# Performance work log

Measured on AMD Instinct MI355X. Metric: run time of the kernel, lower is better.

Reference implementation:

```python
import jax, jax.numpy as jnp
import numpy as np

C = 256
NUM_HEADS = 4
GROUPS = 8
EPS = 1e-5


def setup_inputs() -> dict:
    key = jax.random.key(0)
    ks = jax.random.split(key, 7)
    B, H, W = 4, 64, 64
    x = jax.random.normal(ks[0], (B, C, H, W), dtype=jnp.float32)
    # GroupNorm affine params
    norm_w = jnp.ones((C,), dtype=jnp.float32)
    norm_b = jnp.zeros((C,), dtype=jnp.float32)
    # 1x1 convs == channel-mixing matrices
    qkv_w = jax.random.normal(ks[1], (3 * C, C), dtype=jnp.float32) * (C ** -0.5)
    qkv_b = jnp.zeros((3 * C,), dtype=jnp.float32)
    proj_w = jax.random.normal(ks[2], (C, C), dtype=jnp.float32) * (C ** -0.5)
    proj_b = jnp.zeros((C,), dtype=jnp.float32)
    return {"x": x, "norm_w": norm_w, "norm_b": norm_b,
            "qkv_w": qkv_w, "qkv_b": qkv_b,
            "proj_w": proj_w, "proj_b": proj_b}


def _group_norm(x, w, b):
    B, Cc, H, W = x.shape
    xr = x.reshape(B, GROUPS, Cc // GROUPS, H * W)
    mean = xr.mean(axis=(2, 3), keepdims=True)
    var = xr.var(axis=(2, 3), keepdims=True)
    xn = ((xr - mean) * jax.lax.rsqrt(var + EPS)).reshape(B, Cc, H, W)
    return xn * w[None, :, None, None] + b[None, :, None, None]


def reference(x, norm_w, norm_b, qkv_w, qkv_b, proj_w, proj_b):
    B, Cc, H, W = x.shape
    nh = NUM_HEADS
    d = Cc // nh
    h = _group_norm(x, norm_w, norm_b)
    # 1x1 conv: channel matmul
    qkv = jnp.einsum('oc,bchw->bohw', qkv_w, h) + qkv_b[None, :, None, None]
    q, k, v = jnp.split(qkv, 3, axis=1)
    q = q.reshape(B, nh, d, H * W)
    k = k.reshape(B, nh, d, H * W)
    v = v.reshape(B, nh, d, H * W)
    scale = d ** -0.5
    attn = jnp.einsum('bhci,bhcj->bhij', q, k) * scale  # [B, nh, HW, HW]
    attn = jax.nn.softmax(attn, axis=-1)
    o = jnp.einsum('bhij,bhcj->bhci', attn, v).reshape(B, Cc, H, W)
    out = jnp.einsum('oc,bchw->bohw', proj_w, o) + proj_b[None, :, None, None]
    return x + out
```

## Files before the change

### kernel.cpp

```cpp
#include <hip/hip_runtime.h>

typedef unsigned short u16;
typedef __attribute__((ext_vector_type(8))) short bf16x8;
typedef __attribute__((ext_vector_type(16))) float f32x16;
typedef __attribute__((ext_vector_type(2))) int i32x2;

#define MFMA32(A, B, C) __builtin_amdgcn_mfma_f32_32x32x16_bf16((A), (B), (C), 0, 0, 0)
#define MFMA16(A, B, C) __builtin_amdgcn_mfma_f32_16x16x32_bf16((A), (B), (C), 0, 0, 0)

#define BB 4
#define CC 256
#define HW 4096
#define NH 4
#define HD 64

#define QSCALE 0.18033688f

typedef __attribute__((ext_vector_type(4))) float f32x4;

__device__ __forceinline__ u16 f2bf(float f) {
  unsigned int u = __builtin_bit_cast(unsigned int, f);
  u += 0x7fffu + ((u >> 16) & 1u);
  return (u16)(u >> 16);
}

__device__ __forceinline__ unsigned cvtpk(float a, float b) {
  unsigned r;
  asm("v_cvt_pk_bf16_f32 %0, %1, %2" : "=v"(r) : "v"(a), "v"(b));
  return r;
}

__device__ __forceinline__ uint4 pack_oct(const f32x16& a, int oct, float scl) {
  const int b8 = oct * 8;
  unsigned A0 = cvtpk(a[b8 + 0] * scl, a[b8 + 1] * scl);
  unsigned A1 = cvtpk(a[b8 + 2] * scl, a[b8 + 3] * scl);
  unsigned B0 = cvtpk(a[b8 + 4] * scl, a[b8 + 5] * scl);
  unsigned B1 = cvtpk(a[b8 + 6] * scl, a[b8 + 7] * scl);
  i32x2 r0 = __builtin_amdgcn_permlane32_swap((int)A0, (int)B0, false, false);
  i32x2 r1 = __builtin_amdgcn_permlane32_swap((int)A1, (int)B1, false, false);
  union { unsigned w[4]; uint4 v; } u;
  u.w[0] = (unsigned)r0[0]; u.w[1] = (unsigned)r1[0];
  u.w[2] = (unsigned)r0[1]; u.w[3] = (unsigned)r1[1];
  return u.v;
}

__global__ __launch_bounds__(256) void w2bf_kernel(const float* __restrict__ qw,
                                                   const float* __restrict__ pw,
                                                   u16* __restrict__ wbf) {
  int idx = (blockIdx.x * 256 + threadIdx.x) * 4;
  const int NQ = 768 * 256;
  const float* src = (idx < NQ) ? (qw + idx) : (pw + (idx - NQ));
  float4 v = *(const float4*)src;
  union { u16 u[4]; uint2 w; } pk;
  pk.u[0] = f2bf(v.x); pk.u[1] = f2bf(v.y);
  pk.u[2] = f2bf(v.z); pk.u[3] = f2bf(v.w);
  *(uint2*)(wbf + idx) = pk.w;
}

__global__ __launch_bounds__(256) void gn_partial_kernel(const float* __restrict__ x,
                                                         float* __restrict__ partial) {
  const float4* p = (const float4*)(x + (size_t)blockIdx.x * 16384);
  float s = 0.f, ss = 0.f;
  for (int i = threadIdx.x; i < 4096; i += 256) {
    float4 v = p[i];
    s += (v.x + v.y) + (v.z + v.w);
    ss += (v.x * v.x + v.y * v.y) + (v.z * v.z + v.w * v.w);
  }
#pragma unroll
  for (int msk = 32; msk; msk >>= 1) {
    s += __shfl_xor(s, msk);
    ss += __shfl_xor(ss, msk);
  }
  __shared__ float red[2][4];
  int wave = threadIdx.x >> 6;
  if ((threadIdx.x & 63) == 0) { red[0][wave] = s; red[1][wave] = ss; }
  __syncthreads();
  if (threadIdx.x == 0) {
    partial[blockIdx.x] = red[0][0] + red[0][1] + red[0][2] + red[0][3];
    partial[256 + blockIdx.x] = red[1][0] + red[1][1] + red[1][2] + red[1][3];
  }
}

__global__ __launch_bounds__(64) void gn_final_kernel(const float* __restrict__ partial,
                                                      float* __restrict__ stats) {
  int bg = threadIdx.x;
  if (bg < 32) {
    float S = 0.f, SS = 0.f;
#pragma unroll
    for (int sp = 0; sp < 8; ++sp) {
      S += partial[bg * 8 + sp];
      SS += partial[256 + bg * 8 + sp];
    }
    const float invN = 1.0f / 131072.0f;
    float mean = S * invN;
    float var = SS * invN - mean * mean;
    stats[bg] = mean;
    stats[32 + bg] = rsqrtf(var + 1e-5f);
  }
}

__global__ __launch_bounds__(256) void norm_t_kernel(const float* __restrict__ x,
                                                     const float* __restrict__ nw,
                                                     const float* __restrict__ nb,
                                                     const float* __restrict__ stats,
                                                     u16* __restrict__ h_t) {
  int b = blockIdx.y;
  int s = blockIdx.x * 64 + (threadIdx.x & 63);
  int w = threadIdx.x >> 6;
  const float* xb = x + (size_t)b * CC * HW;
  u16* hb = h_t + ((size_t)b * HW + s) * CC;
#pragma unroll
  for (int cc = 0; cc < 8; ++cc) {
    int c0 = w * 64 + cc * 8;
    union { u16 u[8]; uint4 v; } pk;
#pragma unroll
    for (int j = 0; j < 8; ++j) {
      int c = c0 + j;
      int g = c >> 5;
      float mean = stats[b * 8 + g];
      float rstd = stats[32 + b * 8 + g];
      float a = nw[c] * rstd;
      float bb2 = nb[c] - mean * a;
      float vv = xb[(size_t)c * HW + s];
      pk.u[j] = f2bf(vv * a + bb2);
    }
    *(uint4*)(hb + c0) = pk.v;
  }
}

__global__ __launch_bounds__(256) void qkv_kernel(const u16* __restrict__ h_t,
                                                  const u16* __restrict__ wbf,
                                                  const float* __restrict__ qb,
                                                  u16* __restrict__ q_f,
                                                  u16* __restrict__ k_f,
                                                  u16* __restrict__ v_f) {
  int b = blockIdx.z;
  int y = blockIdx.y;
  int lane = threadIdx.x & 63, wave = threadIdx.x >> 6;
  int ql = lane & 31, hi = lane >> 5;
  int s0w = blockIdx.x * 128 + (wave >> 1) * 64;
  int o0w = y * 128 + (wave & 1) * 64;
  bool isV = (y >= 4);
  const u16* hb = h_t + (size_t)b * HW * CC;

  f32x16 acc[2][2];
  if (!isV) {
#pragma unroll
    for (int mo = 0; mo < 2; ++mo)
#pragma unroll
      for (int r = 0; r < 16; ++r) {
        int row = (r & 3) + 8 * (r >> 2) + 4 * hi;
        float bv = qb[o0w + mo * 32 + row];
        acc[mo][0][r] = bv;
        acc[mo][1][r] = bv;
      }
  } else {
#pragma unroll
    for (int ns = 0; ns < 2; ++ns) {
      float bv = qb[o0w + ns * 32 + ql];
#pragma unroll
      for (int r = 0; r < 16; ++r) {
        acc[0][ns][r] = bv;
        acc[1][ns][r] = bv;
      }
    }
  }

  for (int kk = 0; kk < 16; ++kk) {
    int k0 = kk * 16 + hi * 8;
    bf16x8 wf[2], hf[2];
#pragma unroll
    for (int t = 0; t < 2; ++t) {
      wf[t] = *(const bf16x8*)(wbf + (size_t)(o0w + t * 32 + ql) * CC + k0);
      hf[t] = *(const bf16x8*)(hb + (size_t)(s0w + t * 32 + ql) * CC + k0);
    }
    if (!isV) {
      acc[0][0] = MFMA32(wf[0], hf[0], acc[0][0]);
      acc[0][1] = MFMA32(wf[0], hf[1], acc[0][1]);
      acc[1][0] = MFMA32(wf[1], hf[0], acc[1][0]);
      acc[1][1] = MFMA32(wf[1], hf[1], acc[1][1]);
    } else {
      acc[0][0] = MFMA32(hf[0], wf[0], acc[0][0]);
      acc[0][1] = MFMA32(hf[0], wf[1], acc[0][1]);
      acc[1][0] = MFMA32(hf[1], wf[0], acc[1][0]);
      acc[1][1] = MFMA32(hf[1], wf[1], acc[1][1]);
    }
  }

  if (!isV) {
    bool isQ = (y < 2);
    float scl = isQ ? QSCALE : 1.0f;
    int headL = (o0w >> 6) - (isQ ? 0 : 4);
    u16* base = (isQ ? q_f : k_f) + (size_t)(b * NH + headL) * HW * HD;
#pragma unroll
    for (int mo = 0; mo < 2; ++mo)
#pragma unroll
      for (int ns = 0; ns < 2; ++ns) {
        int s32 = (s0w >> 5) + ns;
#pragma unroll
        for (int oct = 0; oct < 2; ++oct) {
          int kc = mo * 2 + oct;
          uint4 v = pack_oct(acc[mo][ns], oct, scl);
          *(uint4*)(base + ((size_t)(s32 * 4 + kc) * 64 + lane) * 8) = v;
        }
      }
  } else {
    int headv = (o0w >> 6) - 8;
    u16* base = v_f + (size_t)(b * NH + headv) * HW * HD;
#pragma unroll
    for (int mo = 0; mo < 2; ++mo)
#pragma unroll
      for (int ns = 0; ns < 2; ++ns)
#pragma unroll
        for (int oct = 0; oct < 2; ++oct) {
          int kvb = s0w + mo * 32 + oct * 16;
          int jb64 = kvb >> 6, kcv = (kvb & 63) >> 4;
          uint4 v = pack_oct(acc[mo][ns], oct, 1.0f);
          *(uint4*)(base + ((size_t)((jb64 * 2 + ns) * 4 + kcv) * 64 + lane) * 8) = v;
        }
  }
}

__global__ __launch_bounds__(512) void attn_kernel(const u16* __restrict__ q_f,
                                                   const u16* __restrict__ k_f,
                                                   const u16* __restrict__ v_f,
                                                   u16* __restrict__ o_t) {
  __shared__ float mbuf[4 * 33 * 64];
  int wgid = blockIdx.x + gridDim.x * blockIdx.y;
  int xcd = wgid & 7;
  int j = wgid >> 3;
  int bh = (xcd << 1) | (j & 1);
  int qblk = j >> 1;
  int tid = threadIdx.x;
  int wave = tid >> 6, lane = tid & 63;
  int half = wave >> 2, wsub = wave & 3;
  int ql = lane & 31, hi = lane >> 5;
  int q0w = qblk * 128 + wsub * 32;
  const u16* qfb = q_f + (size_t)bh * HW * HD + lane * 8;
  const u16* kfb = k_f + (size_t)bh * HW * HD + lane * 8;
  const u16* vfb = v_f + (size_t)bh * HW * HD + lane * 8;

  int s32q = q0w >> 5;
  bf16x8 qf[4];
#pragma unroll
  for (int kc = 0; kc < 4; ++kc)
    qf[kc] = *(const bf16x8*)(qfb + (size_t)(s32q * 4 + kc) * 512);

  float l_run = 0.f;
  f32x16 of0 = {}, of1 = {};
  bf16x8 kfr[8], vfr[8];

  {
    const u16* kb = kfb + (size_t)half * 4096;
    const u16* vb = vfb + (size_t)half * 4096;
#pragma unroll
    for (int kc = 0; kc < 4; ++kc) {
      kfr[kc] = *(const bf16x8*)(kb + (size_t)kc * 512);
      kfr[4 + kc] = *(const bf16x8*)(kb + (size_t)(4 + kc) * 512);
      vfr[kc] = *(const bf16x8*)(vb + (size_t)kc * 512);
      vfr[4 + kc] = *(const bf16x8*)(vb + (size_t)(4 + kc) * 512);
    }
  }

#pragma unroll 1
  for (int it = half; it < 64; it += 2) {
    f32x16 s0 = {}, s1 = {};
    __builtin_amdgcn_s_setprio(1);
#pragma unroll
    for (int kc = 0; kc < 4; ++kc) {
      s0 = MFMA32(kfr[kc], qf[kc], s0);
      s1 = MFMA32(kfr[4 + kc], qf[kc], s1);
    }
    __builtin_amdgcn_s_setprio(0);

    {
      const u16* kb = kfb + (size_t)(it + 2) * 4096;
#pragma unroll
      for (int kc = 0; kc < 4; ++kc) {
        kfr[kc] = *(const bf16x8*)(kb + (size_t)kc * 512);
        kfr[4 + kc] = *(const bf16x8*)(kb + (size_t)(4 + kc) * 512);
      }
    }

#pragma unroll
    for (int i = 0; i < 16; ++i) {
      s0[i] = __builtin_amdgcn_exp2f(s0[i]);
      s1[i] = __builtin_amdgcn_exp2f(s1[i]);
    }

    bf16x8 pf[4];
#pragma unroll
    for (int kc = 0; kc < 4; ++kc) {
      const f32x16 pv = (kc < 2) ? s0 : s1;
      const int b8 = (kc & 1) * 8;
      unsigned A0 = cvtpk(pv[b8 + 0], pv[b8 + 1]);
      unsigned A1 = cvtpk(pv[b8 + 2], pv[b8 + 3]);
      unsigned B0 = cvtpk(pv[b8 + 4], pv[b8 + 5]);
      unsigned B1 = cvtpk(pv[b8 + 6], pv[b8 + 7]);
      i32x2 r0 = __builtin_amdgcn_permlane32_swap((int)A0, (int)B0, false, false);
      i32x2 r1 = __builtin_amdgcn_permlane32_swap((int)A1, (int)B1, false, false);
      union { unsigned w[4]; bf16x8 v8; } u;
      u.w[0] = (unsigned)r0[0]; u.w[1] = (unsigned)r1[0];
      u.w[2] = (unsigned)r0[1]; u.w[3] = (unsigned)r1[1];
      pf[kc] = u.v8;
    }

    __builtin_amdgcn_s_setprio(1);
#pragma unroll
    for (int kc = 0; kc < 4; ++kc) {
      of0 = MFMA32(vfr[kc], pf[kc], of0);
      of1 = MFMA32(vfr[4 + kc], pf[kc], of1);
    }
    __builtin_amdgcn_s_setprio(0);

    {
      const u16* vb = vfb + (size_t)(it + 2) * 4096;
#pragma unroll
      for (int kc = 0; kc < 4; ++kc) {
        vfr[kc] = *(const bf16x8*)(vb + (size_t)kc * 512);
        vfr[4 + kc] = *(const bf16x8*)(vb + (size_t)(4 + kc) * 512);
      }
    }

    float t8[8];
#pragma unroll
    for (int i = 0; i < 8; ++i)
      t8[i] = (s0[i] + s0[i + 8]) + (s1[i] + s1[i + 8]);
    float t4a = t8[0] + t8[4], t4b = t8[1] + t8[5];
    float t4c = t8[2] + t8[6], t4d = t8[3] + t8[7];
    l_run += (t4a + t4b) + (t4c + t4d);
  }

  __syncthreads();
  if (half == 1) {
    float* mb = mbuf + (size_t)wsub * 33 * 64 + lane;
#pragma unroll
    for (int i = 0; i < 16; ++i) mb[i * 64] = of0[i];
#pragma unroll
    for (int i = 0; i < 16; ++i) mb[(16 + i) * 64] = of1[i];
    mb[32 * 64] = l_run;
  }
  __syncthreads();
  if (half == 0) {
    const float* mb = mbuf + (size_t)wsub * 33 * 64 + lane;
#pragma unroll
    for (int i = 0; i < 16; ++i) of0[i] += mb[i * 64];
#pragma unroll
    for (int i = 0; i < 16; ++i) of1[i] += mb[(16 + i) * 64];
    l_run += mb[32 * 64];
    float l_tot = l_run + __shfl_xor(l_run, 32);
    float inv_l = 1.0f / l_tot;
    int bb = bh >> 2, hh = bh & 3;
    u16* orow = o_t + ((size_t)bb * HW + q0w + ql) * CC + hh * 64;
#pragma unroll
    for (int cb = 0; cb < 2; ++cb) {
      const f32x16 o = cb ? of1 : of0;
#pragma unroll
      for (int t = 0; t < 4; ++t) {
        int c0 = cb * 32 + t * 8 + hi * 4;
        union { u16 u[4]; uint2 w; } pk;
#pragma unroll
        for (int r = 0; r < 4; ++r) pk.u[r] = f2bf(o[t * 4 + r] * inv_l);
        *(uint2*)(orow + c0) = pk.w;
      }
    }
  }
}

__global__ __launch_bounds__(256) void proj_kernel(const u16* __restrict__ o_t,
                                                   const u16* __restrict__ wbf,
                                                   const float* __restrict__ pb,
                                                   const float* __restrict__ x,
                                                   float* __restrict__ out) {
  int b = blockIdx.z;
  int lane = threadIdx.x & 63, wave = threadIdx.x >> 6;
  int lr = lane & 15, lg = lane >> 4;
  int m0 = blockIdx.x * 128 + (wave >> 1) * 64;
  int n0 = blockIdx.y * 128 + (wave & 1) * 64;
  const u16* ob = o_t + (size_t)b * HW * CC;
  const u16* pwbf = wbf + (size_t)768 * CC;
  f32x4 acc[4][4] = {};
  for (int kc = 0; kc < 8; ++kc) {
    int ko = kc * 32 + lg * 8;
    bf16x8 af[4], bfr[4];
#pragma unroll
    for (int mi = 0; mi < 4; ++mi)
      af[mi] = *(const bf16x8*)(ob + (size_t)(m0 + mi * 16 + lr) * CC + ko);
#pragma unroll
    for (int ni = 0; ni < 4; ++ni)
      bfr[ni] = *(const bf16x8*)(pwbf + (size_t)(n0 + ni * 16 + lr) * CC + ko);
#pragma unroll
    for (int mi = 0; mi < 4; ++mi)
#pragma unroll
      for (int ni = 0; ni < 4; ++ni)
        acc[mi][ni] = MFMA16(af[mi], bfr[ni], acc[mi][ni]);
  }
#pragma unroll
  for (int ni = 0; ni < 4; ++ni) {
    int o = n0 + ni * 16 + lr;
    float bias = pb[o];
    const float* xp = x + ((size_t)b * CC + o) * HW;
    float* op = out + ((size_t)b * CC + o) * HW;
#pragma unroll
    for (int mi = 0; mi < 4; ++mi) {
      int sb = m0 + mi * 16 + lg * 4;
      float4 xv = *(const float4*)(xp + sb);
      float4 res;
      res.x = acc[mi][ni][0] + bias + xv.x;
      res.y = acc[mi][ni][1] + bias + xv.y;
      res.z = acc[mi][ni][2] + bias + xv.z;
      res.w = acc[mi][ni][3] + bias + xv.w;
      *(float4*)(op + sb) = res;
    }
  }
}

extern "C" void kernel_launch(void* const* d_in, const int* in_sizes, int n_in,
                              void* d_out, int out_size, void* d_ws, size_t ws_size,
                              hipStream_t stream) {
  const float* x = (const float*)d_in[0];
  const float* nw = (const float*)d_in[1];
  const float* nb = (const float*)d_in[2];
  const float* qw = (const float*)d_in[3];
  const float* qb = (const float*)d_in[4];
  const float* pw = (const float*)d_in[5];
  const float* pb = (const float*)d_in[6];
  float* out = (float*)d_out;

  float* stats = (float*)d_ws;
  float* partial = stats + 64;
  u16* h_t = (u16*)((char*)d_ws + 4096);
  u16* q_f = h_t + (size_t)BB * HW * CC;
  u16* k_f = q_f + (size_t)BB * HW * CC;
  u16* v_f = k_f + (size_t)BB * HW * CC;
  u16* wbf = v_f + (size_t)BB * HW * CC;
  u16* o_t = h_t;

  gn_partial_kernel<<<256, 256, 0, stream>>>(x, partial);
  gn_final_kernel<<<1, 64, 0, stream>>>(partial, stats);
  w2bf_kernel<<<256, 256, 0, stream>>>(qw, pw, wbf);
  norm_t_kernel<<<dim3(HW / 64, BB), 256, 0, stream>>>(x, nw, nb, stats, h_t);
  qkv_kernel<<<dim3(HW / 128, 6, BB), 256, 0, stream>>>(h_t, wbf, qb, q_f, k_f, v_f);
  attn_kernel<<<dim3(HW / 128, BB * NH), 512, 0, stream>>>(q_f, k_f, v_f, o_t);
  proj_kernel<<<dim3(HW / 128, 2, BB), 256, 0, stream>>>(o_t, wbf, pb, x, out);
}
```

Before: 154.5 us.

## Store weights, normalized input, and attention output in MFMA fragment layout

Weights, the normalized activations and the attention output are now written in a pre-swizzled per-lane MFMA fragment layout, so the qkv and proj GEMMs read contiguous 1KB chunks per wave instead of strided rows. norm_t now goes through an LDS transpose, and attention writes its output with packed 16-byte stores. proj switches from 16x16 to 32x32 MFMA and does a scalar-per-lane residual epilogue. The cost is more complex index math, and the proj epilogue now uses 4-byte rather than float4 stores.

```diff
diff --git a/kernel.cpp b/kernel.cpp
--- a/kernel.cpp
+++ b/kernel.cpp
@@ -6,7 +6,6 @@
 typedef __attribute__((ext_vector_type(2))) int i32x2;
 
 #define MFMA32(A, B, C) __builtin_amdgcn_mfma_f32_32x32x16_bf16((A), (B), (C), 0, 0, 0)
-#define MFMA16(A, B, C) __builtin_amdgcn_mfma_f32_16x16x32_bf16((A), (B), (C), 0, 0, 0)
 
 #define BB 4
 #define CC 256
@@ -15,8 +14,6 @@
 #define HD 64
 
 #define QSCALE 0.18033688f
-
-typedef __attribute__((ext_vector_type(4))) float f32x4;
 
 __device__ __forceinline__ u16 f2bf(float f) {
   unsigned int u = __builtin_bit_cast(unsigned int, f);
@@ -46,15 +43,19 @@
 
 __global__ __launch_bounds__(256) void w2bf_kernel(const float* __restrict__ qw,
                                                    const float* __restrict__ pw,
-                                                   u16* __restrict__ wbf) {
-  int idx = (blockIdx.x * 256 + threadIdx.x) * 4;
-  const int NQ = 768 * 256;
-  const float* src = (idx < NQ) ? (qw + idx) : (pw + (idx - NQ));
-  float4 v = *(const float4*)src;
-  union { u16 u[4]; uint2 w; } pk;
-  pk.u[0] = f2bf(v.x); pk.u[1] = f2bf(v.y);
-  pk.u[2] = f2bf(v.z); pk.u[3] = f2bf(v.w);
-  *(uint2*)(wbf + idx) = pk.w;
+                                                   u16* __restrict__ w_f) {
+  int wv = (blockIdx.x * 256 + threadIdx.x) >> 6;
+  int lane = threadIdx.x & 63;
+  int row = (wv >> 4) * 32 + (lane & 31);
+  int c0 = (wv & 15) * 16 + (lane >> 5) * 8;
+  const float* src = (row < 768) ? (qw + (size_t)row * 256 + c0)
+                                 : (pw + (size_t)(row - 768) * 256 + c0);
+  float4 a = *(const float4*)src;
+  float4 b = *(const float4*)(src + 4);
+  union { u16 u[8]; uint4 v; } pk;
+  pk.u[0] = f2bf(a.x); pk.u[1] = f2bf(a.y); pk.u[2] = f2bf(a.z); pk.u[3] = f2bf(a.w);
+  pk.u[4] = f2bf(b.x); pk.u[5] = f2bf(b.y); pk.u[6] = f2bf(b.z); pk.u[7] = f2bf(b.w);
+  *(uint4*)(w_f + ((size_t)wv * 64 + lane) * 8) = pk.v;
 }
 
 __global__ __launch_bounds__(256) void gn_partial_kernel(const float* __restrict__ x,
@@ -103,33 +104,39 @@
                                                      const float* __restrict__ nw,
                                                      const float* __restrict__ nb,
                                                      const float* __restrict__ stats,
-                                                     u16* __restrict__ h_t) {
+                                                     u16* __restrict__ h_f) {
+  __shared__ u16 L[256][66];
   int b = blockIdx.y;
-  int s = blockIdx.x * 64 + (threadIdx.x & 63);
-  int w = threadIdx.x >> 6;
+  int s0 = blockIdx.x * 64;
+  int lane = threadIdx.x & 63, w = threadIdx.x >> 6;
   const float* xb = x + (size_t)b * CC * HW;
-  u16* hb = h_t + ((size_t)b * HW + s) * CC;
-#pragma unroll
-  for (int cc = 0; cc < 8; ++cc) {
-    int c0 = w * 64 + cc * 8;
+  for (int cc = 0; cc < 64; ++cc) {
+    int c = w * 64 + cc;
+    int g = c >> 5;
+    float mean = stats[b * 8 + g];
+    float rstd = stats[32 + b * 8 + g];
+    float a = nw[c] * rstd;
+    float b2 = nb[c] - mean * a;
+    float v = xb[(size_t)c * HW + s0 + lane];
+    L[c][lane] = f2bf(v * a + b2);
+  }
+  __syncthreads();
+  u16* hb = h_f + (size_t)b * HW * CC;
+  int ql = lane & 31, hi = lane >> 5;
+  for (int t = w; t < 32; t += 4) {
+    int s32t = t >> 4, kc = t & 15;
+    int c0 = kc * 16 + hi * 8;
+    int s = s32t * 32 + ql;
     union { u16 u[8]; uint4 v; } pk;
 #pragma unroll
-    for (int j = 0; j < 8; ++j) {
-      int c = c0 + j;
-      int g = c >> 5;
-      float mean = stats[b * 8 + g];
-      float rstd = stats[32 + b * 8 + g];
-      float a = nw[c] * rstd;
-      float bb2 = nb[c] - mean * a;
-      float vv = xb[(size_t)c * HW + s];
-      pk.u[j] = f2bf(vv * a + bb2);
-    }
-    *(uint4*)(hb + c0) = pk.v;
-  }
-}
-
-__global__ __launch_bounds__(256) void qkv_kernel(const u16* __restrict__ h_t,
-                                                  const u16* __restrict__ wbf,
+    for (int j = 0; j < 8; ++j) pk.u[j] = L[c0 + j][s];
+    int s32g = (s0 >> 5) + s32t;
+    *(uint4*)(hb + ((size_t)(s32g * 16 + kc) * 64 + lane) * 8) = pk.v;
+  }
+}
+
+__global__ __launch_bounds__(256) void qkv_kernel(const u16* __restrict__ h_f,
+                                                  const u16* __restrict__ w_f,
                                                   const float* __restrict__ qb,
                                                   u16* __restrict__ q_f,
                                                   u16* __restrict__ k_f,
@@ -141,7 +148,7 @@
   int s0w = blockIdx.x * 128 + (wave >> 1) * 64;
   int o0w = y * 128 + (wave & 1) * 64;
   bool isV = (y >= 4);
-  const u16* hb = h_t + (size_t)b * HW * CC;
+  const u16* hb = h_f + (size_t)b * HW * CC;
 
   f32x16 acc[2][2];
   if (!isV) {
@@ -166,13 +173,13 @@
     }
   }
 
+  int os32 = o0w >> 5, ss32 = s0w >> 5;
   for (int kk = 0; kk < 16; ++kk) {
-    int k0 = kk * 16 + hi * 8;
     bf16x8 wf[2], hf[2];
 #pragma unroll
     for (int t = 0; t < 2; ++t) {
-      wf[t] = *(const bf16x8*)(wbf + (size_t)(o0w + t * 32 + ql) * CC + k0);
-      hf[t] = *(const bf16x8*)(hb + (size_t)(s0w + t * 32 + ql) * CC + k0);
+      wf[t] = *(const bf16x8*)(w_f + ((size_t)((os32 + t) * 16 + kk) * 64 + lane) * 8);
+      hf[t] = *(const bf16x8*)(hb + ((size_t)((ss32 + t) * 16 + kk) * 64 + lane) * 8);
     }
     if (!isV) {
       acc[0][0] = MFMA32(wf[0], hf[0], acc[0][0]);
@@ -196,7 +203,7 @@
     for (int mo = 0; mo < 2; ++mo)
 #pragma unroll
       for (int ns = 0; ns < 2; ++ns) {
-        int s32 = (s0w >> 5) + ns;
+        int s32 = ss32 + ns;
 #pragma unroll
         for (int oct = 0; oct < 2; ++oct) {
           int kc = mo * 2 + oct;
@@ -224,7 +231,7 @@
 __global__ __launch_bounds__(512) void attn_kernel(const u16* __restrict__ q_f,
                                                    const u16* __restrict__ k_f,
                                                    const u16* __restrict__ v_f,
-                                                   u16* __restrict__ o_t) {
+                                                   u16* __restrict__ o_f) {
   __shared__ float mbuf[4 * 33 * 64];
   int wgid = blockIdx.x + gridDim.x * blockIdx.y;
   int xcd = wgid & 7;
@@ -351,68 +358,68 @@
     float l_tot = l_run + __shfl_xor(l_run, 32);
     float inv_l = 1.0f / l_tot;
     int bb = bh >> 2, hh = bh & 3;
-    u16* orow = o_t + ((size_t)bb * HW + q0w + ql) * CC + hh * 64;
+    u16* obase = o_f + (size_t)bb * HW * CC;
+    int q32 = q0w >> 5;
 #pragma unroll
     for (int cb = 0; cb < 2; ++cb) {
       const f32x16 o = cb ? of1 : of0;
 #pragma unroll
-      for (int t = 0; t < 4; ++t) {
-        int c0 = cb * 32 + t * 8 + hi * 4;
-        union { u16 u[4]; uint2 w; } pk;
-#pragma unroll
-        for (int r = 0; r < 4; ++r) pk.u[r] = f2bf(o[t * 4 + r] * inv_l);
-        *(uint2*)(orow + c0) = pk.w;
-      }
-    }
-  }
-}
-
-__global__ __launch_bounds__(256) void proj_kernel(const u16* __restrict__ o_t,
-                                                   const u16* __restrict__ wbf,
+      for (int oct = 0; oct < 2; ++oct) {
+        int ck = hh * 4 + cb * 2 + oct;
+        uint4 v = pack_oct(o, oct, inv_l);
+        *(uint4*)(obase + ((size_t)(q32 * 16 + ck) * 64 + lane) * 8) = v;
+      }
+    }
+  }
+}
+
+__global__ __launch_bounds__(256) void proj_kernel(const u16* __restrict__ o_f,
+                                                   const u16* __restrict__ w_f,
                                                    const float* __restrict__ pb,
                                                    const float* __restrict__ x,
                                                    float* __restrict__ out) {
   int b = blockIdx.z;
   int lane = threadIdx.x & 63, wave = threadIdx.x >> 6;
-  int lr = lane & 15, lg = lane >> 4;
-  int m0 = blockIdx.x * 128 + (wave >> 1) * 64;
-  int n0 = blockIdx.y * 128 + (wave & 1) * 64;
-  const u16* ob = o_t + (size_t)b * HW * CC;
-  const u16* pwbf = wbf + (size_t)768 * CC;
-  f32x4 acc[4][4] = {};
-  for (int kc = 0; kc < 8; ++kc) {
-    int ko = kc * 32 + lg * 8;
-    bf16x8 af[4], bfr[4];
-#pragma unroll
-    for (int mi = 0; mi < 4; ++mi)
-      af[mi] = *(const bf16x8*)(ob + (size_t)(m0 + mi * 16 + lr) * CC + ko);
-#pragma unroll
-    for (int ni = 0; ni < 4; ++ni)
-      bfr[ni] = *(const bf16x8*)(pwbf + (size_t)(n0 + ni * 16 + lr) * CC + ko);
-#pragma unroll
-    for (int mi = 0; mi < 4; ++mi)
-#pragma unroll
-      for (int ni = 0; ni < 4; ++ni)
-        acc[mi][ni] = MFMA16(af[mi], bfr[ni], acc[mi][ni]);
-  }
-#pragma unroll
-  for (int ni = 0; ni < 4; ++ni) {
-    int o = n0 + ni * 16 + lr;
-    float bias = pb[o];
-    const float* xp = x + ((size_t)b * CC + o) * HW;
-    float* op = out + ((size_t)b * CC + o) * HW;
-#pragma unroll
-    for (int mi = 0; mi < 4; ++mi) {
-      int sb = m0 + mi * 16 + lg * 4;
-      float4 xv = *(const float4*)(xp + sb);
-      float4 res;
-      res.x = acc[mi][ni][0] + bias + xv.x;
-      res.y = acc[mi][ni][1] + bias + xv.y;
-      res.z = acc[mi][ni][2] + bias + xv.z;
-      res.w = acc[mi][ni][3] + bias + xv.w;
-      *(float4*)(op + sb) = res;
-    }
-  }
+  int ql = lane & 31, hi = lane >> 5;
+  int s0w = blockIdx.x * 128 + (wave >> 1) * 64;
+  int o0w = blockIdx.y * 128 + (wave & 1) * 64;
+  const u16* ob = o_f + (size_t)b * HW * CC;
+
+  f32x16 acc[2][2];
+#pragma unroll
+  for (int mo = 0; mo < 2; ++mo)
+#pragma unroll
+    for (int r = 0; r < 16; ++r) {
+      int row = (r & 3) + 8 * (r >> 2) + 4 * hi;
+      float bv = pb[o0w + mo * 32 + row];
+      acc[mo][0][r] = bv;
+      acc[mo][1][r] = bv;
+    }
+
+  int os32 = 24 + (o0w >> 5), ss32 = s0w >> 5;
+  for (int kk = 0; kk < 16; ++kk) {
+    bf16x8 af[2], bf2[2];
+#pragma unroll
+    for (int t = 0; t < 2; ++t) {
+      af[t] = *(const bf16x8*)(w_f + ((size_t)((os32 + t) * 16 + kk) * 64 + lane) * 8);
+      bf2[t] = *(const bf16x8*)(ob + ((size_t)((ss32 + t) * 16 + kk) * 64 + lane) * 8);
+    }
+    acc[0][0] = MFMA32(af[0], bf2[0], acc[0][0]);
+    acc[0][1] = MFMA32(af[0], bf2[1], acc[0][1]);
+    acc[1][0] = MFMA32(af[1], bf2[0], acc[1][0]);
+    acc[1][1] = MFMA32(af[1], bf2[1], acc[1][1]);
+  }
+
+#pragma unroll
+  for (int mo = 0; mo < 2; ++mo)
+#pragma unroll
+    for (int r = 0; r < 16; ++r) {
+      int o = o0w + mo * 32 + (r & 3) + 8 * (r >> 2) + 4 * hi;
+      const float* xp = x + ((size_t)b * CC + o) * HW + s0w + ql;
+      float* op = out + ((size_t)b * CC + o) * HW + s0w + ql;
+      op[0] = acc[mo][0][r] + xp[0];
+      op[32] = acc[mo][1][r] + xp[32];
+    }
 }
 
 extern "C" void kernel_launch(void* const* d_in, const int* in_sizes, int n_in,
@@ -429,18 +436,18 @@
 
   float* stats = (float*)d_ws;
   float* partial = stats + 64;
-  u16* h_t = (u16*)((char*)d_ws + 4096);
-  u16* q_f = h_t + (size_t)BB * HW * CC;
+  u16* h_f = (u16*)((char*)d_ws + 4096);
+  u16* q_f = h_f + (size_t)BB * HW * CC;
   u16* k_f = q_f + (size_t)BB * HW * CC;
   u16* v_f = k_f + (size_t)BB * HW * CC;
-  u16* wbf = v_f + (size_t)BB * HW * CC;
-  u16* o_t = h_t;
+  u16* w_f = v_f + (size_t)BB * HW * CC;
+  u16* o_f = h_f;
 
   gn_partial_kernel<<<256, 256, 0, stream>>>(x, partial);
   gn_final_kernel<<<1, 64, 0, stream>>>(partial, stats);
-  w2bf_kernel<<<256, 256, 0, stream>>>(qw, pw, wbf);
-  norm_t_kernel<<<dim3(HW / 64, BB), 256, 0, stream>>>(x, nw, nb, stats, h_t);
-  qkv_kernel<<<dim3(HW / 128, 6, BB), 256, 0, stream>>>(h_t, wbf, qb, q_f, k_f, v_f);
-  attn_kernel<<<dim3(HW / 128, BB * NH), 512, 0, stream>>>(q_f, k_f, v_f, o_t);
-  proj_kernel<<<dim3(HW / 128, 2, BB), 256, 0, stream>>>(o_t, wbf, pb, x, out);
-}
+  w2bf_kernel<<<128, 256, 0, stream>>>(qw, pw, w_f);
+  norm_t_kernel<<<dim3(HW / 64, BB), 256, 0, stream>>>(x, nw, nb, stats, h_f);
+  qkv_kernel<<<dim3(HW / 128, 6, BB), 256, 0, stream>>>(h_f, w_f, qb, q_f, k_f, v_f);
+  attn_kernel<<<dim3(HW / 128, BB * NH), 512, 0, stream>>>(q_f, k_f, v_f, o_f);
+  proj_kernel<<<dim3(HW / 128, 2, BB), 256, 0, stream>>>(o_f, w_f, pb, x, out);
+}
```

Measured after the change: 139.3 us. 1.11x faster.
